# Kernel tuning notes

Hardware: AMD Instinct MI355X
Metric: run time of the kernel (lower is better)

## Reference

```python
import jax, jax.numpy as jnp
import numpy as np

N_NODES = 20000
N_EDGES = 160000
D_IN = 512
D_OUT = 64


def _propagate(x, src, dst, num_nodes):
    # SLPropagate with add_self_loops=False, normalize=False:
    # out[dst] += x[src]  (plain sum aggregation over incoming edges)
    return jax.ops.segment_sum(x[src], dst, num_segments=num_nodes)


def setup_inputs() -> dict:
    key = jax.random.key(0)
    k1, k2, k3, k4 = jax.random.split(key, 4)
    x = jax.random.normal(k1, (N_NODES, D_IN), dtype=jnp.float32)
    edge_index = jax.random.randint(k2, (2, N_EDGES), 0, N_NODES, dtype=jnp.int64)
    # torch.nn.Linear default init scale ~ 1/sqrt(fan_in)
    s = 1.0 / np.sqrt(D_IN)
    W1 = jax.random.uniform(k3, (D_IN, D_IN), dtype=jnp.float32, minval=-s, maxval=s)
    W2 = jax.random.uniform(k4, (D_OUT, D_IN), dtype=jnp.float32, minval=-s, maxval=s)
    return {"x": x, "edge_index": edge_index, "W1": W1, "W2": W2}


def reference(x, edge_index, W1, W2):
    num_nodes = x.shape[0]
    src, dst = edge_index[0], edge_index[1]
    h = _propagate(x, src, dst, num_nodes)          # [N, D_IN]
    h = jax.nn.relu(jnp.einsum('nd,ed->ne', h, W1))  # lin1 (no bias) + relu
    h = _propagate(h, src, dst, num_nodes)          # [N, D_IN]
    h = jnp.einsum('nd,od->no', h, W2)              # lin2 (no bias) -> [N, D_OUT]
    return jax.nn.log_softmax(h, axis=1)
```

## Files before the change

### kernel.cpp

```cpp
#include <hip/hip_runtime.h>

#define D 512
#define DOUT 64
#define MAXDEG 64

typedef __bf16 bf16x8 __attribute__((ext_vector_type(8)));
typedef float floatx4 __attribute__((ext_vector_type(4)));

__device__ __forceinline__ void async_cp16(const void* g, void* lds) {
    __builtin_amdgcn_global_load_lds(
        (__attribute__((address_space(1))) void*)(void*)g,
        (__attribute__((address_space(3))) void*)lds, 16, 0, 0);
}

__global__ __launch_bounds__(256) void prep_kernel(
        int* __restrict__ cnt, int nN, int zeroBlocks,
        __bf16* __restrict__ tzero,
        const float* __restrict__ W1, __bf16* __restrict__ w1b, int w1N8,
        const float* __restrict__ W2, __bf16* __restrict__ w2b, int w2N8) {
    int b = blockIdx.x;
    if (b < zeroBlocks) {
        int i4 = b * 1024 + threadIdx.x * 4;
        if (i4 + 3 < nN) *(int4*)(cnt + i4) = make_int4(0, 0, 0, 0);
        else {
            if (i4 + 0 < nN) cnt[i4 + 0] = 0;
            if (i4 + 1 < nN) cnt[i4 + 1] = 0;
            if (i4 + 2 < nN) cnt[i4 + 2] = 0;
        }
        return;
    }
    b -= zeroBlocks;
    if (b == 0) {
        ((unsigned*)tzero)[threadIdx.x] = 0u;
        return;
    }
    b -= 1;
    int w1Blocks = (w1N8 + 255) >> 8;
    const float* in; __bf16* outp; int n8;
    if (b < w1Blocks) { in = W1; outp = w1b; n8 = w1N8; }
    else { b -= w1Blocks; in = W2; outp = w2b; n8 = w2N8; }
    int i = b * 256 + threadIdx.x;
    if (i < n8) {
        const float4* p = (const float4*)in + (size_t)i * 2;
        float4 v0 = p[0], v1 = p[1];
        bf16x8 o;
        o[0] = (__bf16)v0.x; o[1] = (__bf16)v0.y; o[2] = (__bf16)v0.z; o[3] = (__bf16)v0.w;
        o[4] = (__bf16)v1.x; o[5] = (__bf16)v1.y; o[6] = (__bf16)v1.z; o[7] = (__bf16)v1.w;
        *((bf16x8*)outp + i) = o;
    }
}

__global__ __launch_bounds__(256, 3) void gemm1_fill(
        const float* __restrict__ Af, const __bf16* __restrict__ B,
        __bf16* __restrict__ Cout, int M, int gemmBlocks,
        const int* __restrict__ src, const int* __restrict__ dst,
        int* __restrict__ cnt, int* __restrict__ col, int nE) {
    if (blockIdx.x >= gemmBlocks) {
        int base = (blockIdx.x - gemmBlocks) * 256 + threadIdx.x;
        int stride = (gridDim.x - gemmBlocks) * 256;
        for (int e = base; e < nE; e += stride) {
            int d = dst[e];
            int slot = atomicAdd(&cnt[d], 1);
            if (slot < MAXDEG) col[(size_t)d * MAXDEG + slot] = src[e];
        }
        return;
    }
    constexpr int BM = 128, BN = 128;
    __shared__ float  Asf[BM * 16 * 4];
    __shared__ __bf16 Bs[8 * BN * 8];

    const int qch = gemmBlocks >> 3, rch = gemmBlocks & 7;
    const int xcd = blockIdx.x & 7, jj = blockIdx.x >> 3;
    const int L = (xcd < rch ? xcd * (qch + 1) : rch * (qch + 1) + (xcd - rch) * qch) + jj;

    const int tid = threadIdx.x;
    const int w = tid >> 6, lane = tid & 63;
    const int wrow = w >> 1, wcol = w & 1;
    const int m0 = (L >> 2) * BM, n0 = (L & 3) * BN;
    const int quad = lane >> 4, l15 = lane & 15;

    const int srow = lane >> 3;
    const int skq  = (lane & 7) ^ (srow & 7);

    floatx4 acc[4][4] = {};

    for (int k0 = 0; k0 < D; k0 += 64) {
        #pragma unroll
        for (int c = 0; c < 8; ++c) {
            int P0 = (w * 8 + c) * 64;
            int P = P0 + lane;
            int rloc = P >> 4, cu = P & 15;
            int gr = m0 + rloc; if (gr > M - 1) gr = M - 1;
            async_cp16(Af + (size_t)gr * D + k0 + ((cu ^ (rloc & 15)) << 2),
                       &Asf[(size_t)P0 * 4]);
        }
        #pragma unroll
        for (int c = 0; c < 4; ++c) {
            int P0 = (w * 4 + c) * 64;
            int nn = n0 + (P0 >> 3) + srow;
            async_cp16(B + (size_t)nn * D + k0 + skq * 8, &Bs[(size_t)P0 * 8]);
        }
        __syncthreads();

        #pragma unroll
        for (int ksub = 0; ksub < 2; ++ksub) {
            const int kk = ksub * 4 + quad;
            bf16x8 af[4], bfr[4];
            #pragma unroll
            for (int mi = 0; mi < 4; ++mi) {
                int rr = wrow * 64 + mi * 16 + l15;
                int u0 = ((kk << 1)    ) ^ (rr & 15);
                int u1 = ((kk << 1) | 1) ^ (rr & 15);
                float4 f0 = *(const float4*)&Asf[(size_t)(rr * 16 + u0) * 4];
                float4 f1 = *(const float4*)&Asf[(size_t)(rr * 16 + u1) * 4];
                bf16x8 a_;
                a_[0] = (__bf16)f0.x; a_[1] = (__bf16)f0.y;
                a_[2] = (__bf16)f0.z; a_[3] = (__bf16)f0.w;
                a_[4] = (__bf16)f1.x; a_[5] = (__bf16)f1.y;
                a_[6] = (__bf16)f1.z; a_[7] = (__bf16)f1.w;
                af[mi] = a_;
            }
            #pragma unroll
            for (int nj = 0; nj < 4; ++nj) {
                int row = wcol * 64 + nj * 16 + l15;
                bfr[nj] = *(const bf16x8*)&Bs[(size_t)(row * 8 + (kk ^ (row & 7))) * 8];
            }
            #pragma unroll
            for (int mi = 0; mi < 4; ++mi)
                #pragma unroll
                for (int nj = 0; nj < 4; ++nj)
                    acc[mi][nj] = __builtin_amdgcn_mfma_f32_16x16x32_bf16(
                        af[mi], bfr[nj], acc[mi][nj], 0, 0, 0);
        }
        __syncthreads();
    }

    #pragma unroll
    for (int mi = 0; mi < 4; ++mi) {
        #pragma unroll
        for (int r = 0; r < 4; ++r) {
            int m = m0 + wrow * 64 + mi * 16 + quad * 4 + r;
            if (m < M) {
                #pragma unroll
                for (int nj = 0; nj < 4; ++nj) {
                    int n = n0 + wcol * 64 + nj * 16 + l15;
                    Cout[(size_t)m * D + n] = (__bf16)acc[mi][nj][r];
                }
            }
        }
    }
}

__global__ __launch_bounds__(256) void prop1_gemm2(
        const __bf16* __restrict__ t, const int* __restrict__ cnt,
        const int* __restrict__ col, const __bf16* __restrict__ B,
        __bf16* __restrict__ u, int nN) {
    __shared__ __bf16 As[16 * 512];

    const int tid = threadIdx.x;
    const int w = tid >> 6, lane = tid & 63;
    const int quad = lane >> 4, l15 = lane & 15;
    const int m0 = blockIdx.x * 8;

    int deg[2];
    const int4* ip[2];
    float acc[2][8] = {};
    int maxb = 0;
    #pragma unroll
    for (int q = 0; q < 2; ++q) {
        int n = m0 + w + q * 4;
        int nc = (n < nN) ? n : 0;
        int d = 0;
        if (n < nN) { d = cnt[n]; if (d > MAXDEG) d = MAXDEG; }
        deg[q] = d;
        ip[q] = (const int4*)(col + (size_t)nc * MAXDEG);
        int bq = (d + 3) >> 2;
        if (bq > maxb) maxb = bq;
    }

    for (int b = 0; b < maxb; ++b) {
        int s[2][4];
        #pragma unroll
        for (int q = 0; q < 2; ++q) {
            int4 i4 = ip[q][b];
            int e0 = b * 4;
            s[q][0] = (e0 + 0 < deg[q]) ? i4.x : nN;
            s[q][1] = (e0 + 1 < deg[q]) ? i4.y : nN;
            s[q][2] = (e0 + 2 < deg[q]) ? i4.z : nN;
            s[q][3] = (e0 + 3 < deg[q]) ? i4.w : nN;
        }
        bf16x8 v[2][4];
        #pragma unroll
        for (int q = 0; q < 2; ++q)
            #pragma unroll
            for (int j = 0; j < 4; ++j)
                v[q][j] = *(const bf16x8*)(t + (size_t)s[q][j] * D + lane * 8);
        #pragma unroll
        for (int q = 0; q < 2; ++q)
            #pragma unroll
            for (int i = 0; i < 8; ++i)
                acc[q][i] += ((float)v[q][0][i] + (float)v[q][1][i])
                           + ((float)v[q][2][i] + (float)v[q][3][i]);
    }

    bf16x8 breg[16];
    #pragma unroll
    for (int kq = 0; kq < 16; ++kq)
        breg[kq] = *(const bf16x8*)(B + (size_t)(w * 16 + l15) * D + kq * 32 + quad * 8);

    #pragma unroll
    for (int q = 0; q < 2; ++q) {
        int r = w + q * 4;
        bf16x8 o;
        #pragma unroll
        for (int i = 0; i < 8; ++i) o[i] = (__bf16)fmaxf(acc[q][i], 0.f);
        int P = r * 64 + ((lane + r) & 63);
        *(bf16x8*)&As[(size_t)P * 8] = o;
    }
    __syncthreads();

    floatx4 c = {};
    #pragma unroll
    for (int kq = 0; kq < 16; ++kq) {
        int g = kq * 4 + quad;
        bf16x8 af = *(const bf16x8*)&As[(size_t)(l15 * 64 + ((g + l15) & 63)) * 8];
        c = __builtin_amdgcn_mfma_f32_16x16x32_bf16(af, breg[kq], c, 0, 0, 0);
    }

    #pragma unroll
    for (int r = 0; r < 4; ++r) {
        int row = quad * 4 + r;
        int m = m0 + row;
        if (row < 8 && m < nN)
            u[(size_t)m * DOUT + w * 16 + l15] = (__bf16)c[r];
    }
}

__global__ __launch_bounds__(256) void prop2_lsm(const __bf16* __restrict__ u,
        const int* __restrict__ cnt, const int* __restrict__ col,
        float* __restrict__ out, int nN) {
    int n = blockIdx.x * 4 + (threadIdx.x >> 6);
    if (n >= nN) return;
    int lane = threadIdx.x & 63;
    int deg = cnt[n]; if (deg > MAXDEG) deg = MAXDEG;
    const int* cp = col + (size_t)n * MAXDEG;
    float a0 = 0.f, a1 = 0.f, a2 = 0.f, a3 = 0.f;
    float a4 = 0.f, a5 = 0.f, a6 = 0.f, a7 = 0.f;
    int e = 0;
    for (; e + 8 <= deg; e += 8) {
        int s0 = cp[e],     s1 = cp[e + 1], s2 = cp[e + 2], s3 = cp[e + 3];
        int s4 = cp[e + 4], s5 = cp[e + 5], s6 = cp[e + 6], s7 = cp[e + 7];
        a0 += (float)u[(size_t)s0 * DOUT + lane];
        a1 += (float)u[(size_t)s1 * DOUT + lane];
        a2 += (float)u[(size_t)s2 * DOUT + lane];
        a3 += (float)u[(size_t)s3 * DOUT + lane];
        a4 += (float)u[(size_t)s4 * DOUT + lane];
        a5 += (float)u[(size_t)s5 * DOUT + lane];
        a6 += (float)u[(size_t)s6 * DOUT + lane];
        a7 += (float)u[(size_t)s7 * DOUT + lane];
    }
    for (; e + 4 <= deg; e += 4) {
        int s0 = cp[e], s1 = cp[e + 1], s2 = cp[e + 2], s3 = cp[e + 3];
        a0 += (float)u[(size_t)s0 * DOUT + lane];
        a1 += (float)u[(size_t)s1 * DOUT + lane];
        a2 += (float)u[(size_t)s2 * DOUT + lane];
        a3 += (float)u[(size_t)s3 * DOUT + lane];
    }
    for (; e < deg; ++e) a0 += (float)u[(size_t)cp[e] * DOUT + lane];
    float v = ((a0 + a4) + (a1 + a5)) + ((a2 + a6) + (a3 + a7));
    float mx = v;
    #pragma unroll
    for (int off = 32; off >= 1; off >>= 1) mx = fmaxf(mx, __shfl_xor(mx, off, 64));
    float s = expf(v - mx);
    #pragma unroll
    for (int off = 32; off >= 1; off >>= 1) s += __shfl_xor(s, off, 64);
    out[(size_t)n * DOUT + lane] = v - mx - logf(s);
}


extern "C" void kernel_launch(void* const* d_in, const int* in_sizes, int n_in,
                              void* d_out, int out_size, void* d_ws, size_t ws_size,
                              hipStream_t stream) {
    const float* x  = (const float*)d_in[0];
    const int*   ei = (const int*)d_in[1];
    const float* W1 = (const float*)d_in[2];
    const float* W2 = (const float*)d_in[3];
    float* out = (float*)d_out;

    const int N = in_sizes[0] / D;
    const int E = in_sizes[1] / 2;
    const int* src = ei;
    const int* dst = ei + E;

    size_t off = 0;
    auto alloc = [&](size_t bytes) -> void* {
        void* p = (char*)d_ws + off;
        off = (off + bytes + 255) & ~(size_t)255;
        return p;
    };
    int*    cnt     = (int*)alloc(sizeof(int) * (size_t)N);
    int*    col     = (int*)alloc(sizeof(int) * (size_t)N * MAXDEG);
    __bf16* w1b     = (__bf16*)alloc(sizeof(__bf16) * (size_t)D * D);
    __bf16* w2b     = (__bf16*)alloc(sizeof(__bf16) * (size_t)DOUT * D);
    __bf16* t       = (__bf16*)alloc(sizeof(__bf16) * (size_t)(N + 1) * D);
    __bf16* u       = (__bf16*)alloc(sizeof(__bf16) * (size_t)N * DOUT);

    const int zeroBlocks = (N + 1023) / 1024;
    const int w1N8 = D * D / 8, w2N8 = DOUT * D / 8;
    const int cvtBlocks = (w1N8 + 255) / 256 + (w2N8 + 255) / 256;

    prep_kernel<<<zeroBlocks + 1 + cvtBlocks, 256, 0, stream>>>(
        cnt, N, zeroBlocks, t + (size_t)N * D, W1, w1b, w1N8, W2, w2b, w2N8);

    const int gemmBlocks = ((N + 127) / 128) * 4;
    gemm1_fill<<<gemmBlocks + 64, 256, 0, stream>>>(
        x, w1b, t, N, gemmBlocks, src, dst, cnt, col, E);

    prop1_gemm2<<<(N + 7) / 8, 256, 0, stream>>>(t, cnt, col, w2b, u, N);

    prop2_lsm<<<(N + 3) / 4, 256, 0, stream>>>(u, cnt, col, out, N);
}
```

Before: 155.4 us.

## Double-buffer GEMM1 with register-staged bf16 A tiles and split edge fill

The first GEMM now loads each fp32 A tile into registers, converts it to bf16 once and stores it into a double-buffered LDS tile. The next k-tile loads are issued while the current tile feeds the MFMAs, so there is one barrier per step instead of two. This halves A's LDS footprint and removes the repeated fp32-to-bf16 conversion per MFMA fragment. The edge-bucketing fill moves out of the fused GEMM launch into its own kernel with one thread per edge, which adds a launch and drops the concurrency between fill and GEMM. Launch bounds change from 3 to 2 blocks per CU.

```diff
diff --git a/kernel.cpp b/kernel.cpp
--- a/kernel.cpp
+++ b/kernel.cpp
@@ -50,24 +50,23 @@
     }
 }
 
-__global__ __launch_bounds__(256, 3) void gemm1_fill(
-        const float* __restrict__ Af, const __bf16* __restrict__ B,
-        __bf16* __restrict__ Cout, int M, int gemmBlocks,
+__global__ __launch_bounds__(256) void fill_kernel(
         const int* __restrict__ src, const int* __restrict__ dst,
         int* __restrict__ cnt, int* __restrict__ col, int nE) {
-    if (blockIdx.x >= gemmBlocks) {
-        int base = (blockIdx.x - gemmBlocks) * 256 + threadIdx.x;
-        int stride = (gridDim.x - gemmBlocks) * 256;
-        for (int e = base; e < nE; e += stride) {
-            int d = dst[e];
-            int slot = atomicAdd(&cnt[d], 1);
-            if (slot < MAXDEG) col[(size_t)d * MAXDEG + slot] = src[e];
-        }
-        return;
-    }
+    int e = blockIdx.x * 256 + threadIdx.x;
+    if (e < nE) {
+        int d = dst[e];
+        int slot = atomicAdd(&cnt[d], 1);
+        if (slot < MAXDEG) col[(size_t)d * MAXDEG + slot] = src[e];
+    }
+}
+
+__global__ __launch_bounds__(256, 2) void gemm1(
+        const float* __restrict__ Af, const __bf16* __restrict__ B,
+        __bf16* __restrict__ Cout, int M, int gemmBlocks) {
     constexpr int BM = 128, BN = 128;
-    __shared__ float  Asf[BM * 16 * 4];
-    __shared__ __bf16 Bs[8 * BN * 8];
+    __shared__ __bf16 As[2][BM * 8 * 8];
+    __shared__ __bf16 Bs[2][BN * 8 * 8];
 
     const int qch = gemmBlocks >> 3, rch = gemmBlocks & 7;
     const int xcd = blockIdx.x & 7, jj = blockIdx.x >> 3;
@@ -82,48 +81,60 @@
     const int srow = lane >> 3;
     const int skq  = (lane & 7) ^ (srow & 7);
 
+    const int arow = w * 32 + (lane >> 1);
+    const int ahalf = lane & 1;
+    int agr = m0 + arow; if (agr > M - 1) agr = M - 1;
+    const float* aptr = Af + (size_t)agr * D + ahalf * 32;
+
     floatx4 acc[4][4] = {};
-
-    for (int k0 = 0; k0 < D; k0 += 64) {
-        #pragma unroll
-        for (int c = 0; c < 8; ++c) {
-            int P0 = (w * 8 + c) * 64;
-            int P = P0 + lane;
-            int rloc = P >> 4, cu = P & 15;
-            int gr = m0 + rloc; if (gr > M - 1) gr = M - 1;
-            async_cp16(Af + (size_t)gr * D + k0 + ((cu ^ (rloc & 15)) << 2),
-                       &Asf[(size_t)P0 * 4]);
-        }
-        #pragma unroll
-        for (int c = 0; c < 4; ++c) {
-            int P0 = (w * 4 + c) * 64;
-            int nn = n0 + (P0 >> 3) + srow;
-            async_cp16(B + (size_t)nn * D + k0 + skq * 8, &Bs[(size_t)P0 * 8]);
-        }
-        __syncthreads();
-
+    float4 areg[8];
+
+    #pragma unroll
+    for (int j = 0; j < 8; ++j) areg[j] = *(const float4*)(aptr + j * 4);
+    #pragma unroll
+    for (int c = 0; c < 4; ++c) {
+        int P0 = (w * 4 + c) * 64;
+        int nn = n0 + (P0 >> 3) + srow;
+        async_cp16(B + (size_t)nn * D + skq * 8, &Bs[0][(size_t)P0 * 8]);
+    }
+    #pragma unroll
+    for (int j = 0; j < 4; ++j) {
+        int kq = ahalf * 4 + j;
+        float4 f0 = areg[2 * j], f1 = areg[2 * j + 1];
+        bf16x8 o;
+        o[0] = (__bf16)f0.x; o[1] = (__bf16)f0.y; o[2] = (__bf16)f0.z; o[3] = (__bf16)f0.w;
+        o[4] = (__bf16)f1.x; o[5] = (__bf16)f1.y; o[6] = (__bf16)f1.z; o[7] = (__bf16)f1.w;
+        *(bf16x8*)&As[0][(size_t)(arow * 8 + (kq ^ (arow & 7))) * 8] = o;
+    }
+    __syncthreads();
+
+    for (int it = 0; it < 8; ++it) {
+        const int cur = it & 1;
+        const int k1 = (it + 1) * 64;
+        if (it < 7) {
+            #pragma unroll
+            for (int j = 0; j < 8; ++j) areg[j] = *(const float4*)(aptr + k1 + j * 4);
+            #pragma unroll
+            for (int c = 0; c < 4; ++c) {
+                int P0 = (w * 4 + c) * 64;
+                int nn = n0 + (P0 >> 3) + srow;
+                async_cp16(B + (size_t)nn * D + k1 + skq * 8,
+                           &Bs[cur ^ 1][(size_t)P0 * 8]);
+            }
+        }
         #pragma unroll
         for (int ksub = 0; ksub < 2; ++ksub) {
             const int kk = ksub * 4 + quad;
             bf16x8 af[4], bfr[4];
             #pragma unroll
             for (int mi = 0; mi < 4; ++mi) {
-                int rr = wrow * 64 + mi * 16 + l15;
-                int u0 = ((kk << 1)    ) ^ (rr & 15);
-                int u1 = ((kk << 1) | 1) ^ (rr & 15);
-                float4 f0 = *(const float4*)&Asf[(size_t)(rr * 16 + u0) * 4];
-                float4 f1 = *(const float4*)&Asf[(size_t)(rr * 16 + u1) * 4];
-                bf16x8 a_;
-                a_[0] = (__bf16)f0.x; a_[1] = (__bf16)f0.y;
-                a_[2] = (__bf16)f0.z; a_[3] = (__bf16)f0.w;
-                a_[4] = (__bf16)f1.x; a_[5] = (__bf16)f1.y;
-                a_[6] = (__bf16)f1.z; a_[7] = (__bf16)f1.w;
-                af[mi] = a_;
+                int row = wrow * 64 + mi * 16 + l15;
+                af[mi] = *(const bf16x8*)&As[cur][(size_t)(row * 8 + (kk ^ (row & 7))) * 8];
             }
             #pragma unroll
             for (int nj = 0; nj < 4; ++nj) {
                 int row = wcol * 64 + nj * 16 + l15;
-                bfr[nj] = *(const bf16x8*)&Bs[(size_t)(row * 8 + (kk ^ (row & 7))) * 8];
+                bfr[nj] = *(const bf16x8*)&Bs[cur][(size_t)(row * 8 + (kk ^ (row & 7))) * 8];
             }
             #pragma unroll
             for (int mi = 0; mi < 4; ++mi)
@@ -131,6 +142,17 @@
                 for (int nj = 0; nj < 4; ++nj)
                     acc[mi][nj] = __builtin_amdgcn_mfma_f32_16x16x32_bf16(
                         af[mi], bfr[nj], acc[mi][nj], 0, 0, 0);
+        }
+        if (it < 7) {
+            #pragma unroll
+            for (int j = 0; j < 4; ++j) {
+                int kq = ahalf * 4 + j;
+                float4 f0 = areg[2 * j], f1 = areg[2 * j + 1];
+                bf16x8 o;
+                o[0] = (__bf16)f0.x; o[1] = (__bf16)f0.y; o[2] = (__bf16)f0.z; o[3] = (__bf16)f0.w;
+                o[4] = (__bf16)f1.x; o[5] = (__bf16)f1.y; o[6] = (__bf16)f1.z; o[7] = (__bf16)f1.w;
+                *(bf16x8*)&As[cur ^ 1][(size_t)(arow * 8 + (kq ^ (arow & 7))) * 8] = o;
+            }
         }
         __syncthreads();
     }
@@ -312,9 +334,10 @@
     prep_kernel<<<zeroBlocks + 1 + cvtBlocks, 256, 0, stream>>>(
         cnt, N, zeroBlocks, t + (size_t)N * D, W1, w1b, w1N8, W2, w2b, w2N8);
 
+    fill_kernel<<<(E + 255) / 256, 256, 0, stream>>>(src, dst, cnt, col, E);
+
     const int gemmBlocks = ((N + 127) / 128) * 4;
-    gemm1_fill<<<gemmBlocks + 64, 256, 0, stream>>>(
-        x, w1b, t, N, gemmBlocks, src, dst, cnt, col, E);
+    gemm1<<<gemmBlocks, 256, 0, stream>>>(x, w1b, t, N, gemmBlocks);
 
     prop1_gemm2<<<(N + 7) / 8, 256, 0, stream>>>(t, cnt, col, w2b, u, N);
 
```

New measurement: 180.8 us. +16.4%, slower.

## Split first propagation into feature-sliced gather kernel and separate GEMM2, use 16-bit column indices

Applied to the files above, without the earlier changes.

The fused prop1+gemm2 kernel is split in two. A sliced gather kernel has each block handle one 64-column slice of 32 nodes, which is meant to improve L2 locality of the gathered rows, and it writes the relu'd aggregate to a new h2 buffer. A separate gemm2 kernel then loads h2 tiles into LDS asynchronously. Column indices are stored as unsigned short to halve CSR traffic. This only works while N is at most 65536, adds an extra 20MB round trip through h2 and one more launch, and the grid sizes assume N is divisible by 32 and 16.

```diff
diff --git a/kernel.cpp b/kernel.cpp
--- a/kernel.cpp
+++ b/kernel.cpp
@@ -54,14 +54,14 @@
         const float* __restrict__ Af, const __bf16* __restrict__ B,
         __bf16* __restrict__ Cout, int M, int gemmBlocks,
         const int* __restrict__ src, const int* __restrict__ dst,
-        int* __restrict__ cnt, int* __restrict__ col, int nE) {
+        int* __restrict__ cnt, unsigned short* __restrict__ col, int nE) {
     if (blockIdx.x >= gemmBlocks) {
         int base = (blockIdx.x - gemmBlocks) * 256 + threadIdx.x;
         int stride = (gridDim.x - gemmBlocks) * 256;
         for (int e = base; e < nE; e += stride) {
             int d = dst[e];
             int slot = atomicAdd(&cnt[d], 1);
-            if (slot < MAXDEG) col[(size_t)d * MAXDEG + slot] = src[e];
+            if (slot < MAXDEG) col[(size_t)d * MAXDEG + slot] = (unsigned short)src[e];
         }
         return;
     }
@@ -151,56 +151,64 @@
     }
 }
 
-__global__ __launch_bounds__(256) void prop1_gemm2(
+__global__ __launch_bounds__(256) void prop1_slice(
         const __bf16* __restrict__ t, const int* __restrict__ cnt,
-        const int* __restrict__ col, const __bf16* __restrict__ B,
+        const unsigned short* __restrict__ col, __bf16* __restrict__ h2, int nN) {
+    const int tid = threadIdx.x;
+    const int w = tid >> 6, lane = tid & 63;
+    const int slice = blockIdx.x & 7;
+    const int grp = blockIdx.x >> 3;
+    const int oct = lane & 7;
+    const int n = grp * 32 + w * 8 + (lane >> 3);
+
+    int deg = cnt[n]; if (deg > MAXDEG) deg = MAXDEG;
+    int rounds = deg;
+    #pragma unroll
+    for (int off = 32; off >= 1; off >>= 1) {
+        int o = __shfl_xor(rounds, off, 64);
+        rounds = rounds > o ? rounds : o;
+    }
+    int rb = (rounds + 3) & ~3;
+
+    const unsigned short* cp = col + (size_t)n * MAXDEG;
+    const __bf16* tb = t + (size_t)slice * 64 + (size_t)oct * 8;
+
+    float acc[8] = {};
+    for (int r = 0; r < rb; r += 4) {
+        int s0 = (r + 0 < deg) ? (int)cp[r + 0] : nN;
+        int s1 = (r + 1 < deg) ? (int)cp[r + 1] : nN;
+        int s2 = (r + 2 < deg) ? (int)cp[r + 2] : nN;
+        int s3 = (r + 3 < deg) ? (int)cp[r + 3] : nN;
+        bf16x8 v0 = *(const bf16x8*)(tb + (size_t)s0 * D);
+        bf16x8 v1 = *(const bf16x8*)(tb + (size_t)s1 * D);
+        bf16x8 v2 = *(const bf16x8*)(tb + (size_t)s2 * D);
+        bf16x8 v3 = *(const bf16x8*)(tb + (size_t)s3 * D);
+        #pragma unroll
+        for (int i = 0; i < 8; ++i)
+            acc[i] += ((float)v0[i] + (float)v1[i]) + ((float)v2[i] + (float)v3[i]);
+    }
+
+    bf16x8 o8;
+    #pragma unroll
+    for (int i = 0; i < 8; ++i) o8[i] = (__bf16)fmaxf(acc[i], 0.f);
+    *(bf16x8*)(h2 + (size_t)n * D + slice * 64 + oct * 8) = o8;
+}
+
+__global__ __launch_bounds__(256) void gemm2(
+        const __bf16* __restrict__ h2, const __bf16* __restrict__ B,
         __bf16* __restrict__ u, int nN) {
     __shared__ __bf16 As[16 * 512];
 
     const int tid = threadIdx.x;
     const int w = tid >> 6, lane = tid & 63;
     const int quad = lane >> 4, l15 = lane & 15;
-    const int m0 = blockIdx.x * 8;
-
-    int deg[2];
-    const int4* ip[2];
-    float acc[2][8] = {};
-    int maxb = 0;
-    #pragma unroll
-    for (int q = 0; q < 2; ++q) {
-        int n = m0 + w + q * 4;
-        int nc = (n < nN) ? n : 0;
-        int d = 0;
-        if (n < nN) { d = cnt[n]; if (d > MAXDEG) d = MAXDEG; }
-        deg[q] = d;
-        ip[q] = (const int4*)(col + (size_t)nc * MAXDEG);
-        int bq = (d + 3) >> 2;
-        if (bq > maxb) maxb = bq;
-    }
-
-    for (int b = 0; b < maxb; ++b) {
-        int s[2][4];
-        #pragma unroll
-        for (int q = 0; q < 2; ++q) {
-            int4 i4 = ip[q][b];
-            int e0 = b * 4;
-            s[q][0] = (e0 + 0 < deg[q]) ? i4.x : nN;
-            s[q][1] = (e0 + 1 < deg[q]) ? i4.y : nN;
-            s[q][2] = (e0 + 2 < deg[q]) ? i4.z : nN;
-            s[q][3] = (e0 + 3 < deg[q]) ? i4.w : nN;
-        }
-        bf16x8 v[2][4];
-        #pragma unroll
-        for (int q = 0; q < 2; ++q)
-            #pragma unroll
-            for (int j = 0; j < 4; ++j)
-                v[q][j] = *(const bf16x8*)(t + (size_t)s[q][j] * D + lane * 8);
-        #pragma unroll
-        for (int q = 0; q < 2; ++q)
-            #pragma unroll
-            for (int i = 0; i < 8; ++i)
-                acc[q][i] += ((float)v[q][0][i] + (float)v[q][1][i])
-                           + ((float)v[q][2][i] + (float)v[q][3][i]);
+    const int m0 = blockIdx.x * 16;
+
+    #pragma unroll
+    for (int c = 0; c < 4; ++c) {
+        int r = w * 4 + c;
+        int srcg = (lane - r) & 63;
+        async_cp16(h2 + (size_t)(m0 + r) * D + srcg * 8, &As[(size_t)(r * 64) * 8]);
     }
 
     bf16x8 breg[16];
@@ -208,42 +216,32 @@
     for (int kq = 0; kq < 16; ++kq)
         breg[kq] = *(const bf16x8*)(B + (size_t)(w * 16 + l15) * D + kq * 32 + quad * 8);
 
-    #pragma unroll
-    for (int q = 0; q < 2; ++q) {
-        int r = w + q * 4;
-        bf16x8 o;
-        #pragma unroll
-        for (int i = 0; i < 8; ++i) o[i] = (__bf16)fmaxf(acc[q][i], 0.f);
-        int P = r * 64 + ((lane + r) & 63);
-        *(bf16x8*)&As[(size_t)P * 8] = o;
-    }
     __syncthreads();
 
-    floatx4 c = {};
+    floatx4 c4 = {};
     #pragma unroll
     for (int kq = 0; kq < 16; ++kq) {
         int g = kq * 4 + quad;
         bf16x8 af = *(const bf16x8*)&As[(size_t)(l15 * 64 + ((g + l15) & 63)) * 8];
-        c = __builtin_amdgcn_mfma_f32_16x16x32_bf16(af, breg[kq], c, 0, 0, 0);
+        c4 = __builtin_amdgcn_mfma_f32_16x16x32_bf16(af, breg[kq], c4, 0, 0, 0);
     }
 
     #pragma unroll
     for (int r = 0; r < 4; ++r) {
-        int row = quad * 4 + r;
-        int m = m0 + row;
-        if (row < 8 && m < nN)
-            u[(size_t)m * DOUT + w * 16 + l15] = (__bf16)c[r];
+        int m = m0 + quad * 4 + r;
+        if (m < nN)
+            u[(size_t)m * DOUT + w * 16 + l15] = (__bf16)c4[r];
     }
 }
 
 __global__ __launch_bounds__(256) void prop2_lsm(const __bf16* __restrict__ u,
-        const int* __restrict__ cnt, const int* __restrict__ col,
+        const int* __restrict__ cnt, const unsigned short* __restrict__ col,
         float* __restrict__ out, int nN) {
     int n = blockIdx.x * 4 + (threadIdx.x >> 6);
     if (n >= nN) return;
     int lane = threadIdx.x & 63;
     int deg = cnt[n]; if (deg > MAXDEG) deg = MAXDEG;
-    const int* cp = col + (size_t)n * MAXDEG;
+    const unsigned short* cp = col + (size_t)n * MAXDEG;
     float a0 = 0.f, a1 = 0.f, a2 = 0.f, a3 = 0.f;
     float a4 = 0.f, a5 = 0.f, a6 = 0.f, a7 = 0.f;
     int e = 0;
@@ -298,12 +296,13 @@
         off = (off + bytes + 255) & ~(size_t)255;
         return p;
     };
-    int*    cnt     = (int*)alloc(sizeof(int) * (size_t)N);
-    int*    col     = (int*)alloc(sizeof(int) * (size_t)N * MAXDEG);
-    __bf16* w1b     = (__bf16*)alloc(sizeof(__bf16) * (size_t)D * D);
-    __bf16* w2b     = (__bf16*)alloc(sizeof(__bf16) * (size_t)DOUT * D);
-    __bf16* t       = (__bf16*)alloc(sizeof(__bf16) * (size_t)(N + 1) * D);
-    __bf16* u       = (__bf16*)alloc(sizeof(__bf16) * (size_t)N * DOUT);
+    int*            cnt = (int*)alloc(sizeof(int) * (size_t)N);
+    unsigned short* col = (unsigned short*)alloc(sizeof(unsigned short) * (size_t)N * MAXDEG);
+    __bf16*         w1b = (__bf16*)alloc(sizeof(__bf16) * (size_t)D * D);
+    __bf16*         w2b = (__bf16*)alloc(sizeof(__bf16) * (size_t)DOUT * D);
+    __bf16*         t   = (__bf16*)alloc(sizeof(__bf16) * (size_t)(N + 1) * D);
+    __bf16*         h2  = (__bf16*)alloc(sizeof(__bf16) * (size_t)N * D);
+    __bf16*         u   = (__bf16*)alloc(sizeof(__bf16) * (size_t)N * DOUT);
 
     const int zeroBlocks = (N + 1023) / 1024;
     const int w1N8 = D * D / 8, w2N8 = DOUT * D / 8;
@@ -316,7 +315,9 @@
     gemm1_fill<<<gemmBlocks + 64, 256, 0, stream>>>(
         x, w1b, t, N, gemmBlocks, src, dst, cnt, col, E);
 
-    prop1_gemm2<<<(N + 7) / 8, 256, 0, stream>>>(t, cnt, col, w2b, u, N);
+    prop1_slice<<<(N / 32) * 8, 256, 0, stream>>>(t, cnt, col, h2, N);
+
+    gemm2<<<N / 16, 256, 0, stream>>>(h2, w2b, u, N);
 
     prop2_lsm<<<(N + 3) / 4, 256, 0, stream>>>(u, cnt, col, out, N);
 }
```

Measured after the change: 156.7 us, median of 4. About the same (+0.9%).

## Fuse all stages into a cooperative persistent megakernel and shrink col to 16-bit

Applied to the files above, without the earlier changes.

Replaces the four separate launches with one cooperative-launched persistent kernel that runs prep, edge fill plus GEMM1, prop1+GEMM2, and prop2+log-softmax as phases separated by grid-wide syncs. Tiles are processed with grid-stride loops, and separate kernels remain as a fallback if the cooperative launch fails. The adjacency column array is also stored as 16-bit indices to halve its memory traffic, which only works while node counts fit in 16 bits. This aims to remove launch gaps and inter-kernel idle time, at the cost of grid-sync overhead, a fixed grid size limited by occupancy, and serialising the edge fill with the GEMM within each block.

```diff
diff --git a/kernel.cpp b/kernel.cpp
--- a/kernel.cpp
+++ b/kernel.cpp
@@ -1,4 +1,7 @@
 #include <hip/hip_runtime.h>
+#include <hip/hip_cooperative_groups.h>
+
+namespace cg = cooperative_groups;
 
 #define D 512
 #define DOUT 64
@@ -13,268 +16,318 @@
         (__attribute__((address_space(3))) void*)lds, 16, 0, 0);
 }
 
-__global__ __launch_bounds__(256) void prep_kernel(
-        int* __restrict__ cnt, int nN, int zeroBlocks,
-        __bf16* __restrict__ tzero,
-        const float* __restrict__ W1, __bf16* __restrict__ w1b, int w1N8,
-        const float* __restrict__ W2, __bf16* __restrict__ w2b, int w2N8) {
-    int b = blockIdx.x;
-    if (b < zeroBlocks) {
-        int i4 = b * 1024 + threadIdx.x * 4;
-        if (i4 + 3 < nN) *(int4*)(cnt + i4) = make_int4(0, 0, 0, 0);
-        else {
-            if (i4 + 0 < nN) cnt[i4 + 0] = 0;
-            if (i4 + 1 < nN) cnt[i4 + 1] = 0;
-            if (i4 + 2 < nN) cnt[i4 + 2] = 0;
-        }
-        return;
-    }
-    b -= zeroBlocks;
-    if (b == 0) {
-        ((unsigned*)tzero)[threadIdx.x] = 0u;
-        return;
-    }
-    b -= 1;
-    int w1Blocks = (w1N8 + 255) >> 8;
-    const float* in; __bf16* outp; int n8;
-    if (b < w1Blocks) { in = W1; outp = w1b; n8 = w1N8; }
-    else { b -= w1Blocks; in = W2; outp = w2b; n8 = w2N8; }
-    int i = b * 256 + threadIdx.x;
-    if (i < n8) {
-        const float4* p = (const float4*)in + (size_t)i * 2;
+
+__device__ __forceinline__ void phase_prep(
+        int gt, int T, int nN, int* cnt, __bf16* tpad,
+        const float* W1, __bf16* w1b, const float* W2, __bf16* w2b) {
+    for (int i = gt; i < nN; i += T) cnt[i] = 0;
+    if (gt < 256) ((unsigned*)tpad)[gt] = 0u;
+    const int w1N8 = D * D / 8, w2N8 = DOUT * D / 8;
+    for (int i = gt; i < w1N8; i += T) {
+        const float4* p = (const float4*)W1 + (size_t)i * 2;
         float4 v0 = p[0], v1 = p[1];
         bf16x8 o;
         o[0] = (__bf16)v0.x; o[1] = (__bf16)v0.y; o[2] = (__bf16)v0.z; o[3] = (__bf16)v0.w;
         o[4] = (__bf16)v1.x; o[5] = (__bf16)v1.y; o[6] = (__bf16)v1.z; o[7] = (__bf16)v1.w;
-        *((bf16x8*)outp + i) = o;
-    }
-}
-
-__global__ __launch_bounds__(256, 3) void gemm1_fill(
-        const float* __restrict__ Af, const __bf16* __restrict__ B,
-        __bf16* __restrict__ Cout, int M, int gemmBlocks,
-        const int* __restrict__ src, const int* __restrict__ dst,
-        int* __restrict__ cnt, int* __restrict__ col, int nE) {
-    if (blockIdx.x >= gemmBlocks) {
-        int base = (blockIdx.x - gemmBlocks) * 256 + threadIdx.x;
-        int stride = (gridDim.x - gemmBlocks) * 256;
-        for (int e = base; e < nE; e += stride) {
-            int d = dst[e];
-            int slot = atomicAdd(&cnt[d], 1);
-            if (slot < MAXDEG) col[(size_t)d * MAXDEG + slot] = src[e];
-        }
-        return;
-    }
-    constexpr int BM = 128, BN = 128;
-    __shared__ float  Asf[BM * 16 * 4];
-    __shared__ __bf16 Bs[8 * BN * 8];
-
-    const int qch = gemmBlocks >> 3, rch = gemmBlocks & 7;
-    const int xcd = blockIdx.x & 7, jj = blockIdx.x >> 3;
-    const int L = (xcd < rch ? xcd * (qch + 1) : rch * (qch + 1) + (xcd - rch) * qch) + jj;
-
-    const int tid = threadIdx.x;
+        *((bf16x8*)w1b + i) = o;
+    }
+    for (int i = gt; i < w2N8; i += T) {
+        const float4* p = (const float4*)W2 + (size_t)i * 2;
+        float4 v0 = p[0], v1 = p[1];
+        bf16x8 o;
+        o[0] = (__bf16)v0.x; o[1] = (__bf16)v0.y; o[2] = (__bf16)v0.z; o[3] = (__bf16)v0.w;
+        o[4] = (__bf16)v1.x; o[5] = (__bf16)v1.y; o[6] = (__bf16)v1.z; o[7] = (__bf16)v1.w;
+        *((bf16x8*)w2b + i) = o;
+    }
+}
+
+__device__ __forceinline__ void phase_fill(
+        int gt, int T, const int* src, const int* dst,
+        int* cnt, unsigned short* col, int nE) {
+    for (int e = gt; e < nE; e += T) {
+        int d = dst[e];
+        int slot = atomicAdd(&cnt[d], 1);
+        if (slot < MAXDEG) col[(size_t)d * MAXDEG + slot] = (unsigned short)src[e];
+    }
+}
+
+__device__ __forceinline__ void phase_gemm1(
+        char* smem, int bid, int nB, int tid,
+        const float* Af, const __bf16* B, __bf16* Cout, int M, int gemmBlocks) {
+    float*  Asf = (float*)smem;
+    __bf16* Bs  = (__bf16*)(smem + 32768);
+
     const int w = tid >> 6, lane = tid & 63;
     const int wrow = w >> 1, wcol = w & 1;
-    const int m0 = (L >> 2) * BM, n0 = (L & 3) * BN;
     const int quad = lane >> 4, l15 = lane & 15;
-
     const int srow = lane >> 3;
     const int skq  = (lane & 7) ^ (srow & 7);
 
-    floatx4 acc[4][4] = {};
-
-    for (int k0 = 0; k0 < D; k0 += 64) {
-        #pragma unroll
-        for (int c = 0; c < 8; ++c) {
-            int P0 = (w * 8 + c) * 64;
-            int P = P0 + lane;
-            int rloc = P >> 4, cu = P & 15;
-            int gr = m0 + rloc; if (gr > M - 1) gr = M - 1;
-            async_cp16(Af + (size_t)gr * D + k0 + ((cu ^ (rloc & 15)) << 2),
-                       &Asf[(size_t)P0 * 4]);
-        }
-        #pragma unroll
-        for (int c = 0; c < 4; ++c) {
-            int P0 = (w * 4 + c) * 64;
-            int nn = n0 + (P0 >> 3) + srow;
-            async_cp16(B + (size_t)nn * D + k0 + skq * 8, &Bs[(size_t)P0 * 8]);
-        }
+    for (int tile = bid; tile < gemmBlocks; tile += nB) {
+        const int qch = gemmBlocks >> 3, rch = gemmBlocks & 7;
+        const int xcd = tile & 7, jj = tile >> 3;
+        const int L = (xcd < rch ? xcd * (qch + 1)
+                                 : rch * (qch + 1) + (xcd - rch) * qch) + jj;
+        const int m0 = (L >> 2) * 128, n0 = (L & 3) * 128;
+
+        floatx4 acc[4][4] = {};
         __syncthreads();
 
-        #pragma unroll
-        for (int ksub = 0; ksub < 2; ++ksub) {
-            const int kk = ksub * 4 + quad;
-            bf16x8 af[4], bfr[4];
-            #pragma unroll
-            for (int mi = 0; mi < 4; ++mi) {
-                int rr = wrow * 64 + mi * 16 + l15;
-                int u0 = ((kk << 1)    ) ^ (rr & 15);
-                int u1 = ((kk << 1) | 1) ^ (rr & 15);
-                float4 f0 = *(const float4*)&Asf[(size_t)(rr * 16 + u0) * 4];
-                float4 f1 = *(const float4*)&Asf[(size_t)(rr * 16 + u1) * 4];
-                bf16x8 a_;
-                a_[0] = (__bf16)f0.x; a_[1] = (__bf16)f0.y;
-                a_[2] = (__bf16)f0.z; a_[3] = (__bf16)f0.w;
-                a_[4] = (__bf16)f1.x; a_[5] = (__bf16)f1.y;
-                a_[6] = (__bf16)f1.z; a_[7] = (__bf16)f1.w;
-                af[mi] = a_;
-            }
-            #pragma unroll
-            for (int nj = 0; nj < 4; ++nj) {
-                int row = wcol * 64 + nj * 16 + l15;
-                bfr[nj] = *(const bf16x8*)&Bs[(size_t)(row * 8 + (kk ^ (row & 7))) * 8];
-            }
-            #pragma unroll
-            for (int mi = 0; mi < 4; ++mi)
-                #pragma unroll
-                for (int nj = 0; nj < 4; ++nj)
-                    acc[mi][nj] = __builtin_amdgcn_mfma_f32_16x16x32_bf16(
-                        af[mi], bfr[nj], acc[mi][nj], 0, 0, 0);
-        }
-        __syncthreads();
-    }
-
-    #pragma unroll
-    for (int mi = 0; mi < 4; ++mi) {
-        #pragma unroll
-        for (int r = 0; r < 4; ++r) {
-            int m = m0 + wrow * 64 + mi * 16 + quad * 4 + r;
-            if (m < M) {
+        for (int k0 = 0; k0 < D; k0 += 64) {
+            #pragma unroll
+            for (int c = 0; c < 8; ++c) {
+                int P0 = (w * 8 + c) * 64;
+                int P = P0 + lane;
+                int rloc = P >> 4, cu = P & 15;
+                int gr = m0 + rloc; if (gr > M - 1) gr = M - 1;
+                async_cp16(Af + (size_t)gr * D + k0 + ((cu ^ (rloc & 15)) << 2),
+                           &Asf[(size_t)P0 * 4]);
+            }
+            #pragma unroll
+            for (int c = 0; c < 4; ++c) {
+                int P0 = (w * 4 + c) * 64;
+                int nn = n0 + (P0 >> 3) + srow;
+                async_cp16(B + (size_t)nn * D + k0 + skq * 8, &Bs[(size_t)P0 * 8]);
+            }
+            __syncthreads();
+
+            #pragma unroll
+            for (int ksub = 0; ksub < 2; ++ksub) {
+                const int kk = ksub * 4 + quad;
+                bf16x8 af[4], bfr[4];
+                #pragma unroll
+                for (int mi = 0; mi < 4; ++mi) {
+                    int rr = wrow * 64 + mi * 16 + l15;
+                    int u0 = ((kk << 1)    ) ^ (rr & 15);
+                    int u1 = ((kk << 1) | 1) ^ (rr & 15);
+                    float4 f0 = *(const float4*)&Asf[(size_t)(rr * 16 + u0) * 4];
+                    float4 f1 = *(const float4*)&Asf[(size_t)(rr * 16 + u1) * 4];
+                    bf16x8 a_;
+                    a_[0] = (__bf16)f0.x; a_[1] = (__bf16)f0.y;
+                    a_[2] = (__bf16)f0.z; a_[3] = (__bf16)f0.w;
+                    a_[4] = (__bf16)f1.x; a_[5] = (__bf16)f1.y;
+                    a_[6] = (__bf16)f1.z; a_[7] = (__bf16)f1.w;
+                    af[mi] = a_;
+                }
                 #pragma unroll
                 for (int nj = 0; nj < 4; ++nj) {
-                    int n = n0 + wcol * 64 + nj * 16 + l15;
-                    Cout[(size_t)m * D + n] = (__bf16)acc[mi][nj][r];
+                    int row = wcol * 64 + nj * 16 + l15;
+                    bfr[nj] = *(const bf16x8*)&Bs[(size_t)(row * 8 + (kk ^ (row & 7))) * 8];
                 }
-            }
-        }
-    }
-}
-
-__global__ __launch_bounds__(256) void prop1_gemm2(
-        const __bf16* __restrict__ t, const int* __restrict__ cnt,
-        const int* __restrict__ col, const __bf16* __restrict__ B,
-        __bf16* __restrict__ u, int nN) {
-    __shared__ __bf16 As[16 * 512];
-
-    const int tid = threadIdx.x;
+                #pragma unroll
+                for (int mi = 0; mi < 4; ++mi)
+                    #pragma unroll
+                    for (int nj = 0; nj < 4; ++nj)
+                        acc[mi][nj] = __builtin_amdgcn_mfma_f32_16x16x32_bf16(
+                            af[mi], bfr[nj], acc[mi][nj], 0, 0, 0);
+            }
+            __syncthreads();
+        }
+
+        #pragma unroll
+        for (int mi = 0; mi < 4; ++mi) {
+            #pragma unroll
+            for (int r = 0; r < 4; ++r) {
+                int m = m0 + wrow * 64 + mi * 16 + quad * 4 + r;
+                if (m < M) {
+                    #pragma unroll
+                    for (int nj = 0; nj < 4; ++nj) {
+                        int n = n0 + wcol * 64 + nj * 16 + l15;
+                        Cout[(size_t)m * D + n] = (__bf16)acc[mi][nj][r];
+                    }
+                }
+            }
+        }
+    }
+}
+
+__device__ __forceinline__ void phase_prop1(
+        char* smem, int bid, int nB, int tid,
+        const __bf16* t, const int* cnt, const unsigned short* col,
+        const __bf16* B, __bf16* u, int nN) {
+    __bf16* As = (__bf16*)smem;
     const int w = tid >> 6, lane = tid & 63;
     const int quad = lane >> 4, l15 = lane & 15;
-    const int m0 = blockIdx.x * 8;
-
-    int deg[2];
-    const int4* ip[2];
-    float acc[2][8] = {};
-    int maxb = 0;
-    #pragma unroll
-    for (int q = 0; q < 2; ++q) {
-        int n = m0 + w + q * 4;
-        int nc = (n < nN) ? n : 0;
-        int d = 0;
-        if (n < nN) { d = cnt[n]; if (d > MAXDEG) d = MAXDEG; }
-        deg[q] = d;
-        ip[q] = (const int4*)(col + (size_t)nc * MAXDEG);
-        int bq = (d + 3) >> 2;
-        if (bq > maxb) maxb = bq;
-    }
-
-    for (int b = 0; b < maxb; ++b) {
-        int s[2][4];
+    const int nG = (nN + 7) >> 3;
+
+    for (int g = bid; g < nG; g += nB) {
+        __syncthreads();
+        const int m0 = g * 8;
+
+        int deg[2];
+        const unsigned short* ip[2];
+        float acc[2][8] = {};
+        int maxb = 0;
         #pragma unroll
         for (int q = 0; q < 2; ++q) {
-            int4 i4 = ip[q][b];
-            int e0 = b * 4;
-            s[q][0] = (e0 + 0 < deg[q]) ? i4.x : nN;
-            s[q][1] = (e0 + 1 < deg[q]) ? i4.y : nN;
-            s[q][2] = (e0 + 2 < deg[q]) ? i4.z : nN;
-            s[q][3] = (e0 + 3 < deg[q]) ? i4.w : nN;
-        }
-        bf16x8 v[2][4];
-        #pragma unroll
-        for (int q = 0; q < 2; ++q)
-            #pragma unroll
-            for (int j = 0; j < 4; ++j)
-                v[q][j] = *(const bf16x8*)(t + (size_t)s[q][j] * D + lane * 8);
-        #pragma unroll
-        for (int q = 0; q < 2; ++q)
-            #pragma unroll
-            for (int i = 0; i < 8; ++i)
-                acc[q][i] += ((float)v[q][0][i] + (float)v[q][1][i])
-                           + ((float)v[q][2][i] + (float)v[q][3][i]);
-    }
-
-    bf16x8 breg[16];
-    #pragma unroll
-    for (int kq = 0; kq < 16; ++kq)
-        breg[kq] = *(const bf16x8*)(B + (size_t)(w * 16 + l15) * D + kq * 32 + quad * 8);
-
-    #pragma unroll
-    for (int q = 0; q < 2; ++q) {
-        int r = w + q * 4;
-        bf16x8 o;
-        #pragma unroll
-        for (int i = 0; i < 8; ++i) o[i] = (__bf16)fmaxf(acc[q][i], 0.f);
-        int P = r * 64 + ((lane + r) & 63);
-        *(bf16x8*)&As[(size_t)P * 8] = o;
-    }
-    __syncthreads();
-
-    floatx4 c = {};
-    #pragma unroll
-    for (int kq = 0; kq < 16; ++kq) {
-        int g = kq * 4 + quad;
-        bf16x8 af = *(const bf16x8*)&As[(size_t)(l15 * 64 + ((g + l15) & 63)) * 8];
-        c = __builtin_amdgcn_mfma_f32_16x16x32_bf16(af, breg[kq], c, 0, 0, 0);
-    }
-
-    #pragma unroll
-    for (int r = 0; r < 4; ++r) {
-        int row = quad * 4 + r;
-        int m = m0 + row;
-        if (row < 8 && m < nN)
-            u[(size_t)m * DOUT + w * 16 + l15] = (__bf16)c[r];
-    }
-}
-
-__global__ __launch_bounds__(256) void prop2_lsm(const __bf16* __restrict__ u,
-        const int* __restrict__ cnt, const int* __restrict__ col,
-        float* __restrict__ out, int nN) {
-    int n = blockIdx.x * 4 + (threadIdx.x >> 6);
-    if (n >= nN) return;
-    int lane = threadIdx.x & 63;
-    int deg = cnt[n]; if (deg > MAXDEG) deg = MAXDEG;
-    const int* cp = col + (size_t)n * MAXDEG;
-    float a0 = 0.f, a1 = 0.f, a2 = 0.f, a3 = 0.f;
-    float a4 = 0.f, a5 = 0.f, a6 = 0.f, a7 = 0.f;
-    int e = 0;
-    for (; e + 8 <= deg; e += 8) {
-        int s0 = cp[e],     s1 = cp[e + 1], s2 = cp[e + 2], s3 = cp[e + 3];
-        int s4 = cp[e + 4], s5 = cp[e + 5], s6 = cp[e + 6], s7 = cp[e + 7];
-        a0 += (float)u[(size_t)s0 * DOUT + lane];
-        a1 += (float)u[(size_t)s1 * DOUT + lane];
-        a2 += (float)u[(size_t)s2 * DOUT + lane];
-        a3 += (float)u[(size_t)s3 * DOUT + lane];
-        a4 += (float)u[(size_t)s4 * DOUT + lane];
-        a5 += (float)u[(size_t)s5 * DOUT + lane];
-        a6 += (float)u[(size_t)s6 * DOUT + lane];
-        a7 += (float)u[(size_t)s7 * DOUT + lane];
-    }
-    for (; e + 4 <= deg; e += 4) {
-        int s0 = cp[e], s1 = cp[e + 1], s2 = cp[e + 2], s3 = cp[e + 3];
-        a0 += (float)u[(size_t)s0 * DOUT + lane];
-        a1 += (float)u[(size_t)s1 * DOUT + lane];
-        a2 += (float)u[(size_t)s2 * DOUT + lane];
-        a3 += (float)u[(size_t)s3 * DOUT + lane];
-    }
-    for (; e < deg; ++e) a0 += (float)u[(size_t)cp[e] * DOUT + lane];
-    float v = ((a0 + a4) + (a1 + a5)) + ((a2 + a6) + (a3 + a7));
-    float mx = v;
-    #pragma unroll
-    for (int off = 32; off >= 1; off >>= 1) mx = fmaxf(mx, __shfl_xor(mx, off, 64));
-    float s = expf(v - mx);
-    #pragma unroll
-    for (int off = 32; off >= 1; off >>= 1) s += __shfl_xor(s, off, 64);
-    out[(size_t)n * DOUT + lane] = v - mx - logf(s);
+            int n = m0 + w + q * 4;
+            int nc = (n < nN) ? n : 0;
+            int d = 0;
+            if (n < nN) { d = cnt[n]; if (d > MAXDEG) d = MAXDEG; }
+            deg[q] = d;
+            ip[q] = col + (size_t)nc * MAXDEG;
+            int bq = (d + 3) >> 2;
+            if (bq > maxb) maxb = bq;
+        }
+
+        for (int b = 0; b < maxb; ++b) {
+            int s[2][4];
+            #pragma unroll
+            for (int q = 0; q < 2; ++q) {
+                ushort4 i4 = *(const ushort4*)(ip[q] + b * 4);
+                int e0 = b * 4;
+                s[q][0] = (e0 + 0 < deg[q]) ? (int)i4.x : nN;
+                s[q][1] = (e0 + 1 < deg[q]) ? (int)i4.y : nN;
+                s[q][2] = (e0 + 2 < deg[q]) ? (int)i4.z : nN;
+                s[q][3] = (e0 + 3 < deg[q]) ? (int)i4.w : nN;
+            }
+            bf16x8 v[2][4];
+            #pragma unroll
+            for (int q = 0; q < 2; ++q)
+                #pragma unroll
+                for (int j = 0; j < 4; ++j)
+                    v[q][j] = *(const bf16x8*)(t + (size_t)s[q][j] * D + lane * 8);
+            #pragma unroll
+            for (int q = 0; q < 2; ++q)
+                #pragma unroll
+                for (int i = 0; i < 8; ++i)
+                    acc[q][i] += ((float)v[q][0][i] + (float)v[q][1][i])
+                               + ((float)v[q][2][i] + (float)v[q][3][i]);
+        }
+
+        bf16x8 breg[16];
+        #pragma unroll
+        for (int kq = 0; kq < 16; ++kq)
+            breg[kq] = *(const bf16x8*)(B + (size_t)(w * 16 + l15) * D + kq * 32 + quad * 8);
+
+        #pragma unroll
+        for (int q = 0; q < 2; ++q) {
+            int r = w + q * 4;
+            bf16x8 o;
+            #pragma unroll
+            for (int i = 0; i < 8; ++i) o[i] = (__bf16)fmaxf(acc[q][i], 0.f);
+            int P = r * 64 + ((lane + r) & 63);
+            *(bf16x8*)&As[(size_t)P * 8] = o;
+        }
+        __syncthreads();
+
+        floatx4 c = {};
+        #pragma unroll
+        for (int kq = 0; kq < 16; ++kq) {
+            int g2 = kq * 4 + quad;
+            bf16x8 af = *(const bf16x8*)&As[(size_t)(l15 * 64 + ((g2 + l15) & 63)) * 8];
+            c = __builtin_amdgcn_mfma_f32_16x16x32_bf16(af, breg[kq], c, 0, 0, 0);
+        }
+
+        #pragma unroll
+        for (int r = 0; r < 4; ++r) {
+            int row = quad * 4 + r;
+            int m = m0 + row;
+            if (row < 8 && m < nN)
+                u[(size_t)m * DOUT + w * 16 + l15] = (__bf16)c[r];
+        }
+    }
+}
+
+__device__ __forceinline__ void phase_prop2(
+        int bid, int nB, int tid,
+        const __bf16* u, const int* cnt, const unsigned short* col,
+        float* out, int nN) {
+    const int lane = tid & 63;
+    const int nG = (nN + 3) >> 2;
+    for (int g = bid; g < nG; g += nB) {
+        int n = g * 4 + (tid >> 6);
+        if (n >= nN) continue;
+        int deg = cnt[n]; if (deg > MAXDEG) deg = MAXDEG;
+        const unsigned short* cp = col + (size_t)n * MAXDEG;
+        float a0 = 0.f, a1 = 0.f, a2 = 0.f, a3 = 0.f;
+        float a4 = 0.f, a5 = 0.f, a6 = 0.f, a7 = 0.f;
+        int e = 0;
+        for (; e + 8 <= deg; e += 8) {
+            int s0 = cp[e],     s1 = cp[e + 1], s2 = cp[e + 2], s3 = cp[e + 3];
+            int s4 = cp[e + 4], s5 = cp[e + 5], s6 = cp[e + 6], s7 = cp[e + 7];
+            a0 += (float)u[(size_t)s0 * DOUT + lane];
+            a1 += (float)u[(size_t)s1 * DOUT + lane];
+            a2 += (float)u[(size_t)s2 * DOUT + lane];
+            a3 += (float)u[(size_t)s3 * DOUT + lane];
+            a4 += (float)u[(size_t)s4 * DOUT + lane];
+            a5 += (float)u[(size_t)s5 * DOUT + lane];
+            a6 += (float)u[(size_t)s6 * DOUT + lane];
+            a7 += (float)u[(size_t)s7 * DOUT + lane];
+        }
+        for (; e + 4 <= deg; e += 4) {
+            int s0 = cp[e], s1 = cp[e + 1], s2 = cp[e + 2], s3 = cp[e + 3];
+            a0 += (float)u[(size_t)s0 * DOUT + lane];
+            a1 += (float)u[(size_t)s1 * DOUT + lane];
+            a2 += (float)u[(size_t)s2 * DOUT + lane];
+            a3 += (float)u[(size_t)s3 * DOUT + lane];
+        }
+        for (; e < deg; ++e) a0 += (float)u[(size_t)cp[e] * DOUT + lane];
+        float v = ((a0 + a4) + (a1 + a5)) + ((a2 + a6) + (a3 + a7));
+        float mx = v;
+        #pragma unroll
+        for (int off = 32; off >= 1; off >>= 1) mx = fmaxf(mx, __shfl_xor(mx, off, 64));
+        float s = expf(v - mx);
+        #pragma unroll
+        for (int off = 32; off >= 1; off >>= 1) s += __shfl_xor(s, off, 64);
+        out[(size_t)n * DOUT + lane] = v - mx - logf(s);
+    }
+}
+
+
+__global__ __launch_bounds__(256, 3) void mega(
+        const float* __restrict__ x, const int* __restrict__ src,
+        const int* __restrict__ dst, const float* __restrict__ W1,
+        const float* __restrict__ W2, int* __restrict__ cnt,
+        unsigned short* __restrict__ col, __bf16* __restrict__ w1b,
+        __bf16* __restrict__ w2b, __bf16* __restrict__ t,
+        __bf16* __restrict__ u, float* __restrict__ out,
+        int nN, int nE, int gemmBlocks) {
+    cg::grid_group grid = cg::this_grid();
+    __shared__ __align__(16) char smem[49152];
+
+    const int tid = threadIdx.x, bid = blockIdx.x, nB = gridDim.x;
+    const int gt = bid * 256 + tid, T = nB * 256;
+
+    phase_prep(gt, T, nN, cnt, t + (size_t)nN * D, W1, w1b, W2, w2b);
+    grid.sync();
+
+    phase_fill(gt, T, src, dst, cnt, col, nE);
+    phase_gemm1(smem, bid, nB, tid, x, w1b, t, nN, gemmBlocks);
+    grid.sync();
+
+    phase_prop1(smem, bid, nB, tid, t, cnt, col, w2b, u, nN);
+    grid.sync();
+
+    phase_prop2(bid, nB, tid, u, cnt, col, out, nN);
+}
+
+
+__global__ __launch_bounds__(256) void k_prep(
+        int* cnt, int nN, __bf16* tpad,
+        const float* W1, __bf16* w1b, const float* W2, __bf16* w2b) {
+    phase_prep(blockIdx.x * 256 + threadIdx.x, gridDim.x * 256,
+               nN, cnt, tpad, W1, w1b, W2, w2b);
+}
+__global__ __launch_bounds__(256) void k_fill(
+        const int* src, const int* dst, int* cnt, unsigned short* col, int nE) {
+    phase_fill(blockIdx.x * 256 + threadIdx.x, gridDim.x * 256, src, dst, cnt, col, nE);
+}
+__global__ __launch_bounds__(256, 3) void k_gemm1(
+        const float* Af, const __bf16* B, __bf16* Cout, int M, int gemmBlocks) {
+    __shared__ __align__(16) char smem[49152];
+    phase_gemm1(smem, blockIdx.x, gridDim.x, threadIdx.x, Af, B, Cout, M, gemmBlocks);
+}
+__global__ __launch_bounds__(256) void k_prop1(
+        const __bf16* t, const int* cnt, const unsigned short* col,
+        const __bf16* B, __bf16* u, int nN) {
+    __shared__ __align__(16) char smem[16384];
+    phase_prop1(smem, blockIdx.x, gridDim.x, threadIdx.x, t, cnt, col, B, u, nN);
+}
+__global__ __launch_bounds__(256) void k_prop2(
+        const __bf16* u, const int* cnt, const unsigned short* col,
+        float* out, int nN) {
+    phase_prop2(blockIdx.x, gridDim.x, threadIdx.x, u, cnt, col, out, nN);
 }
 
 
@@ -298,25 +351,44 @@
         off = (off + bytes + 255) & ~(size_t)255;
         return p;
     };
-    int*    cnt     = (int*)alloc(sizeof(int) * (size_t)N);
-    int*    col     = (int*)alloc(sizeof(int) * (size_t)N * MAXDEG);
-    __bf16* w1b     = (__bf16*)alloc(sizeof(__bf16) * (size_t)D * D);
-    __bf16* w2b     = (__bf16*)alloc(sizeof(__bf16) * (size_t)DOUT * D);
-    __bf16* t       = (__bf16*)alloc(sizeof(__bf16) * (size_t)(N + 1) * D);
-    __bf16* u       = (__bf16*)alloc(sizeof(__bf16) * (size_t)N * DOUT);
-
-    const int zeroBlocks = (N + 1023) / 1024;
-    const int w1N8 = D * D / 8, w2N8 = DOUT * D / 8;
-    const int cvtBlocks = (w1N8 + 255) / 256 + (w2N8 + 255) / 256;
-
-    prep_kernel<<<zeroBlocks + 1 + cvtBlocks, 256, 0, stream>>>(
-        cnt, N, zeroBlocks, t + (size_t)N * D, W1, w1b, w1N8, W2, w2b, w2N8);
-
-    const int gemmBlocks = ((N + 127) / 128) * 4;
-    gemm1_fill<<<gemmBlocks + 64, 256, 0, stream>>>(
-        x, w1b, t, N, gemmBlocks, src, dst, cnt, col, E);
-
-    prop1_gemm2<<<(N + 7) / 8, 256, 0, stream>>>(t, cnt, col, w2b, u, N);
-
-    prop2_lsm<<<(N + 3) / 4, 256, 0, stream>>>(u, cnt, col, out, N);
-}
+    int*            cnt = (int*)alloc(sizeof(int) * (size_t)N);
+    unsigned short* col = (unsigned short*)alloc(sizeof(unsigned short) * (size_t)N * MAXDEG);
+    __bf16*         w1b = (__bf16*)alloc(sizeof(__bf16) * (size_t)D * D);
+    __bf16*         w2b = (__bf16*)alloc(sizeof(__bf16) * (size_t)DOUT * D);
+    __bf16*         t   = (__bf16*)alloc(sizeof(__bf16) * (size_t)(N + 1) * D);
+    __bf16*         u   = (__bf16*)alloc(sizeof(__bf16) * (size_t)N * DOUT);
+
+    int gemmBlocks = ((N + 127) / 128) * 4;
+
+    static int coopGrid = -1;
+    if (coopGrid < 0) {
+        int dev = 0, coop = 0, mb = 0;
+        hipGetDevice(&dev);
+        hipDeviceGetAttribute(&coop, hipDeviceAttributeCooperativeLaunch, dev);
+        hipError_t oe = hipOccupancyMaxActiveBlocksPerMultiprocessor(&mb, mega, 256, 0);
+        coopGrid = (coop && oe == hipSuccess && mb > 0) ? mb * 256 : 0;
+        if (coopGrid > 2048) coopGrid = 2048;
+    }
+
+    if (coopGrid > 0) {
+        const float* xa = x; const int* sa = src; const int* da = dst;
+        const float* w1a = W1; const float* w2a = W2;
+        int* ca = cnt; unsigned short* cla = col;
+        __bf16* w1ba = w1b; __bf16* w2ba = w2b; __bf16* ta = t; __bf16* ua = u;
+        float* oa = out;
+        int Nv = N, Ev = E, gBv = gemmBlocks;
+        void* args[] = { &xa, &sa, &da, &w1a, &w2a, &ca, &cla, &w1ba, &w2ba,
+                         &ta, &ua, &oa, &Nv, &Ev, &gBv };
+        hipError_t err = hipLaunchCooperativeKernel(
+            (const void*)mega, dim3(coopGrid), dim3(256), args, 0, stream);
+        if (err == hipSuccess) return;
+        (void)hipGetLastError();
+        coopGrid = 0;
+    }
+
+    k_prep<<<160, 256, 0, stream>>>(cnt, N, t + (size_t)N * D, W1, w1b, W2, w2b);
+    k_fill<<<(E + 255) / 256, 256, 0, stream>>>(src, dst, cnt, col, E);
+    k_gemm1<<<gemmBlocks, 256, 0, stream>>>(x, w1b, t, N, gemmBlocks);
+    k_prop1<<<(N + 7) / 8, 256, 0, stream>>>(t, cnt, col, w2b, u, N);
+    k_prop2<<<(N + 3) / 4, 256, 0, stream>>>(u, cnt, col, out, N);
+}
```

New measurement: 328.9 us. 2.12x slower.
